# Optimization experiments

Hardware: AMD Instinct MI355X
Metric: run time of the kernel (lower is better)

## Reference

```python
import jax, jax.numpy as jnp
import numpy as np

ALPHA = 0.2  # LeakyReLU negative slope
NEG_INF = -9e15  # matches torch's -9000000000000000.0


def setup_inputs() -> dict:
    key = jax.random.key(0)
    k1, k2, k3, k4 = jax.random.split(key, 4)
    B, T, N, F_in, D = 4, 32, 512, 128, 128
    h = jax.random.normal(k1, (B, T, N, F_in), dtype=jnp.float32)
    adj = jax.random.randint(k2, (N, N), 0, 2, dtype=jnp.int32)
    # params: W ~ Linear(in_dim, out_dim, bias=False); a ~ Linear(2*out_dim, 1, bias=False)
    W = jax.random.normal(k3, (F_in, D), dtype=jnp.float32) * 0.05
    a = jax.random.normal(k4, (2 * D,), dtype=jnp.float32) * 0.05
    return {"h": h, "adj": adj, "W": W, "a": a}


def reference(h, adj, W, a):
    # h: (B,T,N,F_in), adj: (N,N), W: (F_in,D), a: (2D,)
    D = W.shape[1]
    Wh = jnp.einsum('btnf,fd->btnd', h, W)  # (B,T,N,D)
    # a . [Wh_i ; Wh_j] == a_src . Wh_i + a_dst . Wh_j -- avoids (N,N,2D) concat
    a_src, a_dst = a[:D], a[D:]
    e_src = Wh @ a_src  # (B,T,N)
    e_dst = Wh @ a_dst  # (B,T,N)
    e = jax.nn.leaky_relu(e_src[..., :, None] + e_dst[..., None, :], ALPHA)  # (B,T,N,N)
    e = jnp.where(adj > 0, e, jnp.float32(NEG_INF))
    attention = jax.nn.softmax(e, axis=-1)  # dropout is identity at eval
    h_prime = jnp.einsum('btij,btjd->btid', attention, Wh)  # (B,T,N,D)
    return h_prime
```

## Files before the change

kernel.cpp:

```cpp
#include <hip/hip_runtime.h>
#include <math.h>

typedef __attribute__((ext_vector_type(8))) short bf16x8;
typedef __attribute__((ext_vector_type(4))) float f32x4;

#define MFMA(a, b, c) __builtin_amdgcn_mfma_f32_16x16x32_bf16(a, b, c, 0, 0, 0)

constexpr int GN = 128;
constexpr int NN = 512;
constexpr int FD = 128;
#define LOG2E 1.4426950408889634f

__device__ inline unsigned rne_top16(float x) {
    unsigned u = __float_as_uint(x);
    return u + 0x7fffu + ((u >> 16) & 1u);
}
__device__ inline unsigned pack_top16(unsigned e1, unsigned e0) {
    return __builtin_amdgcn_perm(e1, e0, 0x07060302u);
}
__device__ inline void gload16(const void* g, void* l) {
    __builtin_amdgcn_global_load_lds(
        (const __attribute__((address_space(1))) unsigned*)g,
        (__attribute__((address_space(3))) unsigned*)l, 16, 0, 0);
}

__global__ __launch_bounds__(256, 2) void whb_kernel(
    const float* __restrict__ h, const float* __restrict__ a,
    const int* __restrict__ adj, const float* __restrict__ W,
    unsigned short* __restrict__ whtHi,
    float* __restrict__ esrc, float* __restrict__ edst,
    unsigned* __restrict__ mask)
{
    __shared__ __attribute__((aligned(16))) unsigned short sW[32768];

    const int bid = blockIdx.x;
    const int xcd = bid & 7, slot = bid >> 3;
    const int g = xcd + 8 * (slot >> 2);
    const int jt = slot & 3;
    const int t = threadIdx.x, lane = t & 63, w = t >> 6;
    const int i0r = jt * 128;
    const int q8 = (lane >> 4) * 8;
    const float* hg = h + (size_t)(g * NN) * FD;

    float4 hv[16];
    #pragma unroll
    for (int kk = 0; kk < 4; ++kk)
        #pragma unroll
        for (int mt = 0; mt < 2; ++mt) {
            const float* src = hg + (size_t)(i0r + w * 32 + mt * 16 + (lane & 15)) * FD
                             + kk * 32 + q8;
            hv[(kk * 2 + mt) * 2 + 0] = *(const float4*)src;
            hv[(kk * 2 + mt) * 2 + 1] = *(const float4*)(src + 4);
        }

    {
        const int pred0 = adj[bid * NN + t] > 0;
        const int pred1 = adj[bid * NN + 256 + t] > 0;
        const unsigned long long m0 = __ballot(pred0);
        const unsigned long long m1 = __ballot(pred1);
        if (lane == 0) {
            mask[bid * 16 + 2 * w]     = (unsigned)m0;
            mask[bid * 16 + 8 + 2 * w] = (unsigned)m1;
        } else if (lane == 1) {
            mask[bid * 16 + 2 * w + 1]     = (unsigned)(m0 >> 32);
            mask[bid * 16 + 8 + 2 * w + 1] = (unsigned)(m1 >> 32);
        }
    }

    #pragma unroll
    for (int grp = 0; grp < 8; ++grp) {
        const int p8 = grp * 256 + t;
        const int lanep = p8 & 63, cn = p8 >> 6;
        const int kks = cn >> 3, nbs = cn & 7;
        const int kbase = kks * 32 + ((lanep >> 4) & 3) * 8;
        const int d = nbs * 16 + (lanep & 15);
        unsigned hi[8], lo[8];
        #pragma unroll
        for (int idx = 0; idx < 8; ++idx) {
            const float wv = W[(kbase + idx) * FD + d];
            const unsigned u = __float_as_uint(wv);
            hi[idx] = u;
            lo[idx] = rne_top16(wv - __uint_as_float(u & 0xffff0000u));
        }
        uint4 H4, L4;
        H4.x = pack_top16(hi[1], hi[0]); H4.y = pack_top16(hi[3], hi[2]);
        H4.z = pack_top16(hi[5], hi[4]); H4.w = pack_top16(hi[7], hi[6]);
        L4.x = pack_top16(lo[1], lo[0]); L4.y = pack_top16(lo[3], lo[2]);
        L4.z = pack_top16(lo[5], lo[4]); L4.w = pack_top16(lo[7], lo[6]);
        *(uint4*)&sW[p8 * 8]         = H4;
        *(uint4*)&sW[16384 + p8 * 8] = L4;
    }
    __syncthreads();

    f32x4 acc[2][8];
    #pragma unroll
    for (int mt = 0; mt < 2; ++mt)
        #pragma unroll
        for (int nb = 0; nb < 8; ++nb) acc[mt][nb] = (f32x4){0.f, 0.f, 0.f, 0.f};

    #pragma unroll
    for (int kk = 0; kk < 4; ++kk) {
        bf16x8 ah[2], al[2];
        #pragma unroll
        for (int mt = 0; mt < 2; ++mt) {
            const float4 f0 = hv[(kk * 2 + mt) * 2 + 0];
            const float4 f1 = hv[(kk * 2 + mt) * 2 + 1];
            const float xs[8] = {f0.x, f0.y, f0.z, f0.w, f1.x, f1.y, f1.z, f1.w};
            union { bf16x8 v; unsigned u[4]; } H, L;
            #pragma unroll
            for (int j = 0; j < 4; ++j) {
                const unsigned e0 = __float_as_uint(xs[2 * j]);
                const unsigned e1 = __float_as_uint(xs[2 * j + 1]);
                H.u[j] = pack_top16(e1, e0);
                const unsigned l0 = rne_top16(xs[2*j]   - __uint_as_float(e0 & 0xffff0000u));
                const unsigned l1 = rne_top16(xs[2*j+1] - __uint_as_float(e1 & 0xffff0000u));
                L.u[j] = pack_top16(l1, l0);
            }
            ah[mt] = H.v; al[mt] = L.v;
        }
        #pragma unroll
        for (int nb = 0; nb < 8; ++nb) {
            const bf16x8 bh = *(const bf16x8*)&sW[((kk * 8 + nb) * 64 + lane) * 8];
            const bf16x8 bl = *(const bf16x8*)&sW[16384 + ((kk * 8 + nb) * 64 + lane) * 8];
            #pragma unroll
            for (int mt = 0; mt < 2; ++mt) {
                acc[mt][nb] = MFMA(al[mt], bh, acc[mt][nb]);
                acc[mt][nb] = MFMA(ah[mt], bl, acc[mt][nb]);
                acc[mt][nb] = MFMA(ah[mt], bh, acc[mt][nb]);
            }
        }
    }

    float av[8], bv[8];
    #pragma unroll
    for (int nb = 0; nb < 8; ++nb) {
        av[nb] = a[nb * 16 + (lane & 15)];
        bv[nb] = a[FD + nb * 16 + (lane & 15)];
    }
    #pragma unroll
    for (int mt = 0; mt < 2; ++mt)
        #pragma unroll
        for (int r = 0; r < 4; ++r) {
            float ps = 0.f, pd = 0.f;
            #pragma unroll
            for (int nb = 0; nb < 8; ++nb) {
                ps += acc[mt][nb][r] * av[nb];
                pd += acc[mt][nb][r] * bv[nb];
            }
            #pragma unroll
            for (int off = 1; off <= 8; off <<= 1) {
                ps += __shfl_xor(ps, off);
                pd += __shfl_xor(pd, off);
            }
            if ((lane & 15) == 0) {
                const int row = g * NN + i0r + w * 32 + mt * 16 + (lane >> 4) * 4 + r;
                esrc[row] = ps;
                edst[row] = pd;
            }
        }

    unsigned short* sT = sW;
    const size_t gbase = (size_t)g * 65536 + (size_t)jt * 16384;
    const int ib = 4 * ((lane >> 4) & 1);

    __syncthreads();
    #pragma unroll
    for (int mt = 0; mt < 2; ++mt) {
        const int lp2 = (lane & 15) + 16 * (mt * 2 + (lane >> 5));
        #pragma unroll
        for (int nb = 0; nb < 8; ++nb) {
            const int off = ((w * 8 + nb) * 64 + lp2) * 8 + ib;
            const unsigned r0 = rne_top16(acc[mt][nb][0]);
            const unsigned r1 = rne_top16(acc[mt][nb][1]);
            const unsigned r2 = rne_top16(acc[mt][nb][2]);
            const unsigned r3 = rne_top16(acc[mt][nb][3]);
            *(uint2*)&sT[off] = make_uint2(pack_top16(r1, r0), pack_top16(r3, r2));
        }
    }
    __syncthreads();
    for (int q = t; q < 2048; q += 256)
        *(float4*)&whtHi[gbase + q * 8] = *(const float4*)&sT[q * 8];
}

__global__ __launch_bounds__(256, 2) void attn_kernel(
    const unsigned short* __restrict__ whtHi,
    const float* __restrict__ esrc, const float* __restrict__ edst,
    const unsigned* __restrict__ mask, float* __restrict__ out)
{
    __shared__ __attribute__((aligned(16))) float eds[NN];
    __shared__ unsigned maskS[128 * 17];
    __shared__ __attribute__((aligned(16))) unsigned short cHi[2][8192];

    const int bid = blockIdx.x;
    const int xcd = bid & 7, slot = bid >> 3;
    const int g = xcd + 8 * (slot >> 2);
    const int it = slot & 3;
    const int t = threadIdx.x, lane = t & 63, w = t >> 6;
    const int i0 = it * 128;
    const int q8 = (lane >> 4) * 8;
    const int l15 = lane & 15;

    eds[t]       = edst[g * NN + t] * LOG2E;
    eds[t + 256] = edst[g * NN + 256 + t] * LOG2E;
    for (int q = t; q < 2048; q += 256) {
        const int row = q >> 4, wo = q & 15;
        maskS[row * 17 + wo] = mask[(i0 + row) * 16 + wo];
    }

    const int rloc0 = w * 32 + l15;
    const int rloc1 = rloc0 + 16;
    const float s0 = esrc[g * NN + i0 + rloc0] * LOG2E;
    const float s1 = esrc[g * NN + i0 + rloc1] * LOG2E;

    union { bf16x8 v; unsigned short s[8]; } bo;
    {
        const unsigned short oneb = (l15 == 0) ? (unsigned short)0x3f80 : (unsigned short)0;
        #pragma unroll
        for (int j = 0; j < 8; ++j) bo.s[j] = oneb;
    }

    const size_t gbase = (size_t)g * 65536;
    for (int q = t; q < 1024; q += 256)
        gload16(&whtHi[gbase + q * 8], &cHi[0][q * 8]);
    __syncthreads();

    f32x4 acc[2][8];
    #pragma unroll
    for (int mt = 0; mt < 2; ++mt)
        #pragma unroll
        for (int nb = 0; nb < 8; ++nb) acc[mt][nb] = (f32x4){0.f, 0.f, 0.f, 0.f};
    f32x4 accS0 = (f32x4){0.f, 0.f, 0.f, 0.f};
    f32x4 accS1 = (f32x4){0.f, 0.f, 0.f, 0.f};

    for (int c2 = 0; c2 < 8; ++c2) {
        const int cur = c2 & 1, nxt = cur ^ 1;
        if (c2 < 7) {
            const size_t gb = gbase + (size_t)(c2 + 1) * 8192;
            for (int q = t; q < 1024; q += 256)
                gload16(&whtHi[gb + q * 8], &cHi[nxt][q * 8]);
        }
        const unsigned short* __restrict__ bHi = &cHi[cur][0];
        #pragma unroll
        for (int kl = 0; kl < 2; ++kl) {
            const int kk = c2 * 2 + kl;
            const float* ep = &eds[kk * 32 + q8];
            const float4 ed0 = *(const float4*)ep;
            const float4 ed1 = *(const float4*)(ep + 4);
            const float ev[8] = {ed0.x, ed0.y, ed0.z, ed0.w, ed1.x, ed1.y, ed1.z, ed1.w};
            const unsigned mw0 = maskS[rloc0 * 17 + kk] >> q8;
            const unsigned mw1 = maskS[rloc1 * 17 + kk] >> q8;

            union { bf16x8 v; unsigned u[4]; } H0, H1;
            unsigned uh0[8], uh1[8];
            #pragma unroll
            for (int i = 0; i < 8; ++i) {
                const float z0 = s0 + ev[i];
                float p0 = __builtin_amdgcn_exp2f(fmaxf(z0, 0.2f * z0));
                p0 = ((mw0 >> i) & 1u) ? p0 : 0.f;
                uh0[i] = __float_as_uint(p0);
                const float z1 = s1 + ev[i];
                float p1 = __builtin_amdgcn_exp2f(fmaxf(z1, 0.2f * z1));
                p1 = ((mw1 >> i) & 1u) ? p1 : 0.f;
                uh1[i] = __float_as_uint(p1);
            }
            #pragma unroll
            for (int j = 0; j < 4; ++j) {
                H0.u[j] = pack_top16(uh0[2*j+1], uh0[2*j]);
                H1.u[j] = pack_top16(uh1[2*j+1], uh1[2*j]);
            }
            #pragma unroll
            for (int nb = 0; nb < 8; ++nb) {
                const bf16x8 bh = *(const bf16x8*)&bHi[((kl * 8 + nb) * 64 + lane) * 8];
                acc[0][nb] = MFMA(H0.v, bh, acc[0][nb]);
                acc[1][nb] = MFMA(H1.v, bh, acc[1][nb]);
            }
            accS0 = MFMA(H0.v, bo.v, accS0);
            accS1 = MFMA(H1.v, bo.v, accS1);
        }
        __syncthreads();
    }

    #pragma unroll
    for (int r = 0; r < 4; ++r) {
        const float rl0 = 1.0f / __shfl(accS0[r], lane & 48);
        const float rl1 = 1.0f / __shfl(accS1[r], lane & 48);
        const int row0 = g * NN + i0 + w * 32 + (lane >> 4) * 4 + r;
        const int row1 = row0 + 16;
        #pragma unroll
        for (int nb = 0; nb < 8; ++nb) {
            out[row0 * FD + nb * 16 + l15] = acc[0][nb][r] * rl0;
            out[row1 * FD + nb * 16 + l15] = acc[1][nb][r] * rl1;
        }
    }
}

extern "C" void kernel_launch(void* const* d_in, const int* in_sizes, int n_in,
                              void* d_out, int out_size, void* d_ws, size_t ws_size,
                              hipStream_t stream) {
    const float* h   = (const float*)d_in[0];
    const int*   adj = (const int*)d_in[1];
    const float* W   = (const float*)d_in[2];
    const float* a   = (const float*)d_in[3];
    float* out = (float*)d_out;

    unsigned short* whtHi = (unsigned short*)d_ws;
    float* esrc = (float*)(whtHi + (size_t)GN * 65536);
    float* edst = esrc + GN * NN;
    unsigned* mask = (unsigned*)(edst + GN * NN);

    whb_kernel<<<512, 256, 0, stream>>>(h, a, adj, W, whtHi, esrc, edst, mask);
    attn_kernel<<<512, 256, 0, stream>>>(whtHi, esrc, edst, mask, out);
}
```

Before: 113.8 us.

## Fuse projection and attention into one kernel with the Wh tile held in LDS

Replaces the two-kernel pipeline with one 512-thread kernel. Each block recomputes the full Wh projection for its graph, keeps it in LDS as bf16 together with the e_src and e_dst scores, then computes attention for half of the rows. The goal is to remove the global round-trip of the bf16 Wh tensor and the score arrays, the separate mask-packing step, and the second launch. In exchange, every graph's projection is computed twice. The adjacency is also read directly as int4 from global memory on every pass. The large LDS footprint (about 148KB) limits the GPU to one block per CU.

```diff
diff --git a/kernel.cpp b/kernel.cpp
--- a/kernel.cpp
+++ b/kernel.cpp
@@ -18,93 +18,69 @@
 __device__ inline unsigned pack_top16(unsigned e1, unsigned e0) {
     return __builtin_amdgcn_perm(e1, e0, 0x07060302u);
 }
-__device__ inline void gload16(const void* g, void* l) {
-    __builtin_amdgcn_global_load_lds(
-        (const __attribute__((address_space(1))) unsigned*)g,
-        (__attribute__((address_space(3))) unsigned*)l, 16, 0, 0);
-}
-
-__global__ __launch_bounds__(256, 2) void whb_kernel(
+
+__global__ __launch_bounds__(512, 2) void gat_fused_kernel(
     const float* __restrict__ h, const float* __restrict__ a,
     const int* __restrict__ adj, const float* __restrict__ W,
-    unsigned short* __restrict__ whtHi,
-    float* __restrict__ esrc, float* __restrict__ edst,
-    unsigned* __restrict__ mask)
+    float* __restrict__ out)
 {
-    __shared__ __attribute__((aligned(16))) unsigned short sW[32768];
+    __shared__ __attribute__((aligned(16))) unsigned short sWh[65536];
+    __shared__ __attribute__((aligned(16))) unsigned short sWc[8192];
+    __shared__ __attribute__((aligned(16))) float sEsrc[NN];
+    __shared__ __attribute__((aligned(16))) float sEdst[NN];
 
     const int bid = blockIdx.x;
     const int xcd = bid & 7, slot = bid >> 3;
-    const int g = xcd + 8 * (slot >> 2);
-    const int jt = slot & 3;
+    const int g  = xcd * 16 + (slot >> 1);
+    const int hf = slot & 1;
     const int t = threadIdx.x, lane = t & 63, w = t >> 6;
-    const int i0r = jt * 128;
-    const int q8 = (lane >> 4) * 8;
-    const float* hg = h + (size_t)(g * NN) * FD;
-
-    float4 hv[16];
-    #pragma unroll
-    for (int kk = 0; kk < 4; ++kk)
-        #pragma unroll
-        for (int mt = 0; mt < 2; ++mt) {
-            const float* src = hg + (size_t)(i0r + w * 32 + mt * 16 + (lane & 15)) * FD
+    const int l15 = lane & 15, q8 = (lane >> 4) * 8;
+    const float* hg = h + (size_t)g * NN * FD;
+
+    f32x4 acc1[4][8];
+    #pragma unroll
+    for (int mt = 0; mt < 4; ++mt)
+        #pragma unroll
+        for (int nb = 0; nb < 8; ++nb) acc1[mt][nb] = (f32x4){0.f, 0.f, 0.f, 0.f};
+
+    const int sd = w * 16 + l15;
+
+    #pragma unroll
+    for (int kk = 0; kk < 4; ++kk) {
+        float4 hv[8];
+        #pragma unroll
+        for (int mt = 0; mt < 4; ++mt) {
+            const float* src = hg + (size_t)(w * 64 + mt * 16 + l15) * FD
                              + kk * 32 + q8;
-            hv[(kk * 2 + mt) * 2 + 0] = *(const float4*)src;
-            hv[(kk * 2 + mt) * 2 + 1] = *(const float4*)(src + 4);
-        }
-
-    {
-        const int pred0 = adj[bid * NN + t] > 0;
-        const int pred1 = adj[bid * NN + 256 + t] > 0;
-        const unsigned long long m0 = __ballot(pred0);
-        const unsigned long long m1 = __ballot(pred1);
-        if (lane == 0) {
-            mask[bid * 16 + 2 * w]     = (unsigned)m0;
-            mask[bid * 16 + 8 + 2 * w] = (unsigned)m1;
-        } else if (lane == 1) {
-            mask[bid * 16 + 2 * w + 1]     = (unsigned)(m0 >> 32);
-            mask[bid * 16 + 8 + 2 * w + 1] = (unsigned)(m1 >> 32);
-        }
-    }
-
-    #pragma unroll
-    for (int grp = 0; grp < 8; ++grp) {
-        const int p8 = grp * 256 + t;
-        const int lanep = p8 & 63, cn = p8 >> 6;
-        const int kks = cn >> 3, nbs = cn & 7;
-        const int kbase = kks * 32 + ((lanep >> 4) & 3) * 8;
-        const int d = nbs * 16 + (lanep & 15);
-        unsigned hi[8], lo[8];
-        #pragma unroll
-        for (int idx = 0; idx < 8; ++idx) {
-            const float wv = W[(kbase + idx) * FD + d];
-            const unsigned u = __float_as_uint(wv);
-            hi[idx] = u;
-            lo[idx] = rne_top16(wv - __uint_as_float(u & 0xffff0000u));
-        }
-        uint4 H4, L4;
-        H4.x = pack_top16(hi[1], hi[0]); H4.y = pack_top16(hi[3], hi[2]);
-        H4.z = pack_top16(hi[5], hi[4]); H4.w = pack_top16(hi[7], hi[6]);
-        L4.x = pack_top16(lo[1], lo[0]); L4.y = pack_top16(lo[3], lo[2]);
-        L4.z = pack_top16(lo[5], lo[4]); L4.w = pack_top16(lo[7], lo[6]);
-        *(uint4*)&sW[p8 * 8]         = H4;
-        *(uint4*)&sW[16384 + p8 * 8] = L4;
-    }
-    __syncthreads();
-
-    f32x4 acc[2][8];
-    #pragma unroll
-    for (int mt = 0; mt < 2; ++mt)
-        #pragma unroll
-        for (int nb = 0; nb < 8; ++nb) acc[mt][nb] = (f32x4){0.f, 0.f, 0.f, 0.f};
-
-    #pragma unroll
-    for (int kk = 0; kk < 4; ++kk) {
-        bf16x8 ah[2], al[2];
-        #pragma unroll
-        for (int mt = 0; mt < 2; ++mt) {
-            const float4 f0 = hv[(kk * 2 + mt) * 2 + 0];
-            const float4 f1 = hv[(kk * 2 + mt) * 2 + 1];
+            hv[2 * mt]     = *(const float4*)src;
+            hv[2 * mt + 1] = *(const float4*)(src + 4);
+        }
+
+        if (kk > 0) __syncthreads();
+        {
+            const int kbase = kk * 32 + q8;
+            unsigned hi[8], lo[8];
+            #pragma unroll
+            for (int idx = 0; idx < 8; ++idx) {
+                const float wv = W[(kbase + idx) * FD + sd];
+                const unsigned u = __float_as_uint(wv);
+                hi[idx] = u;
+                lo[idx] = rne_top16(wv - __uint_as_float(u & 0xffff0000u));
+            }
+            uint4 H4, L4;
+            H4.x = pack_top16(hi[1], hi[0]); H4.y = pack_top16(hi[3], hi[2]);
+            H4.z = pack_top16(hi[5], hi[4]); H4.w = pack_top16(hi[7], hi[6]);
+            L4.x = pack_top16(lo[1], lo[0]); L4.y = pack_top16(lo[3], lo[2]);
+            L4.z = pack_top16(lo[5], lo[4]); L4.w = pack_top16(lo[7], lo[6]);
+            *(uint4*)&sWc[t * 8]        = H4;
+            *(uint4*)&sWc[4096 + t * 8] = L4;
+        }
+        __syncthreads();
+
+        bf16x8 ah[4], al[4];
+        #pragma unroll
+        for (int mt = 0; mt < 4; ++mt) {
+            const float4 f0 = hv[2 * mt], f1 = hv[2 * mt + 1];
             const float xs[8] = {f0.x, f0.y, f0.z, f0.w, f1.x, f1.y, f1.z, f1.w};
             union { bf16x8 v; unsigned u[4]; } H, L;
             #pragma unroll
@@ -120,97 +96,73 @@
         }
         #pragma unroll
         for (int nb = 0; nb < 8; ++nb) {
-            const bf16x8 bh = *(const bf16x8*)&sW[((kk * 8 + nb) * 64 + lane) * 8];
-            const bf16x8 bl = *(const bf16x8*)&sW[16384 + ((kk * 8 + nb) * 64 + lane) * 8];
-            #pragma unroll
-            for (int mt = 0; mt < 2; ++mt) {
-                acc[mt][nb] = MFMA(al[mt], bh, acc[mt][nb]);
-                acc[mt][nb] = MFMA(ah[mt], bl, acc[mt][nb]);
-                acc[mt][nb] = MFMA(ah[mt], bh, acc[mt][nb]);
-            }
-        }
-    }
-
-    float av[8], bv[8];
-    #pragma unroll
-    for (int nb = 0; nb < 8; ++nb) {
-        av[nb] = a[nb * 16 + (lane & 15)];
-        bv[nb] = a[FD + nb * 16 + (lane & 15)];
-    }
-    #pragma unroll
-    for (int mt = 0; mt < 2; ++mt)
-        #pragma unroll
-        for (int r = 0; r < 4; ++r) {
-            float ps = 0.f, pd = 0.f;
+            const bf16x8 bh = *(const bf16x8*)&sWc[(nb * 64 + lane) * 8];
+            const bf16x8 bl = *(const bf16x8*)&sWc[4096 + (nb * 64 + lane) * 8];
+            #pragma unroll
+            for (int mt = 0; mt < 4; ++mt) {
+                acc1[mt][nb] = MFMA(al[mt], bh, acc1[mt][nb]);
+                acc1[mt][nb] = MFMA(ah[mt], bl, acc1[mt][nb]);
+                acc1[mt][nb] = MFMA(ah[mt], bh, acc1[mt][nb]);
+            }
+        }
+    }
+
+    {
+        float av[8], bv[8];
+        #pragma unroll
+        for (int nb = 0; nb < 8; ++nb) {
+            av[nb] = a[nb * 16 + l15];
+            bv[nb] = a[FD + nb * 16 + l15];
+        }
+        #pragma unroll
+        for (int mt = 0; mt < 4; ++mt)
+            #pragma unroll
+            for (int r = 0; r < 4; ++r) {
+                float ps = 0.f, pd = 0.f;
+                #pragma unroll
+                for (int nb = 0; nb < 8; ++nb) {
+                    ps += acc1[mt][nb][r] * av[nb];
+                    pd += acc1[mt][nb][r] * bv[nb];
+                }
+                #pragma unroll
+                for (int off = 1; off <= 8; off <<= 1) {
+                    ps += __shfl_xor(ps, off);
+                    pd += __shfl_xor(pd, off);
+                }
+                if (l15 == 0) {
+                    const int row = w * 64 + mt * 16 + (lane >> 4) * 4 + r;
+                    sEsrc[row] = ps * LOG2E;
+                    sEdst[row] = pd * LOG2E;
+                }
+            }
+    }
+
+    {
+        const int ib = 4 * ((lane >> 4) & 1);
+        #pragma unroll
+        for (int mt = 0; mt < 4; ++mt) {
+            const int KK = w * 2 + (mt >> 1);
+            const int lp2 = l15 + 16 * ((mt & 1) * 2 + (lane >> 5));
             #pragma unroll
             for (int nb = 0; nb < 8; ++nb) {
-                ps += acc[mt][nb][r] * av[nb];
-                pd += acc[mt][nb][r] * bv[nb];
-            }
-            #pragma unroll
-            for (int off = 1; off <= 8; off <<= 1) {
-                ps += __shfl_xor(ps, off);
-                pd += __shfl_xor(pd, off);
-            }
-            if ((lane & 15) == 0) {
-                const int row = g * NN + i0r + w * 32 + mt * 16 + (lane >> 4) * 4 + r;
-                esrc[row] = ps;
-                edst[row] = pd;
-            }
-        }
-
-    unsigned short* sT = sW;
-    const size_t gbase = (size_t)g * 65536 + (size_t)jt * 16384;
-    const int ib = 4 * ((lane >> 4) & 1);
-
+                const int off = ((KK * 8 + nb) * 64 + lp2) * 8 + ib;
+                const unsigned r0 = rne_top16(acc1[mt][nb][0]);
+                const unsigned r1 = rne_top16(acc1[mt][nb][1]);
+                const unsigned r2 = rne_top16(acc1[mt][nb][2]);
+                const unsigned r3 = rne_top16(acc1[mt][nb][3]);
+                *(uint2*)&sWh[off] = make_uint2(pack_top16(r1, r0), pack_top16(r3, r2));
+            }
+        }
+    }
     __syncthreads();
-    #pragma unroll
-    for (int mt = 0; mt < 2; ++mt) {
-        const int lp2 = (lane & 15) + 16 * (mt * 2 + (lane >> 5));
-        #pragma unroll
-        for (int nb = 0; nb < 8; ++nb) {
-            const int off = ((w * 8 + nb) * 64 + lp2) * 8 + ib;
-            const unsigned r0 = rne_top16(acc[mt][nb][0]);
-            const unsigned r1 = rne_top16(acc[mt][nb][1]);
-            const unsigned r2 = rne_top16(acc[mt][nb][2]);
-            const unsigned r3 = rne_top16(acc[mt][nb][3]);
-            *(uint2*)&sT[off] = make_uint2(pack_top16(r1, r0), pack_top16(r3, r2));
-        }
-    }
-    __syncthreads();
-    for (int q = t; q < 2048; q += 256)
-        *(float4*)&whtHi[gbase + q * 8] = *(const float4*)&sT[q * 8];
-}
-
-__global__ __launch_bounds__(256, 2) void attn_kernel(
-    const unsigned short* __restrict__ whtHi,
-    const float* __restrict__ esrc, const float* __restrict__ edst,
-    const unsigned* __restrict__ mask, float* __restrict__ out)
-{
-    __shared__ __attribute__((aligned(16))) float eds[NN];
-    __shared__ unsigned maskS[128 * 17];
-    __shared__ __attribute__((aligned(16))) unsigned short cHi[2][8192];
-
-    const int bid = blockIdx.x;
-    const int xcd = bid & 7, slot = bid >> 3;
-    const int g = xcd + 8 * (slot >> 2);
-    const int it = slot & 3;
-    const int t = threadIdx.x, lane = t & 63, w = t >> 6;
-    const int i0 = it * 128;
-    const int q8 = (lane >> 4) * 8;
-    const int l15 = lane & 15;
-
-    eds[t]       = edst[g * NN + t] * LOG2E;
-    eds[t + 256] = edst[g * NN + 256 + t] * LOG2E;
-    for (int q = t; q < 2048; q += 256) {
-        const int row = q >> 4, wo = q & 15;
-        maskS[row * 17 + wo] = mask[(i0 + row) * 16 + wo];
-    }
 
     const int rloc0 = w * 32 + l15;
-    const int rloc1 = rloc0 + 16;
-    const float s0 = esrc[g * NN + i0 + rloc0] * LOG2E;
-    const float s1 = esrc[g * NN + i0 + rloc1] * LOG2E;
+    const int irow0 = hf * 256 + rloc0;
+    const int irow1 = irow0 + 16;
+    const float s0 = sEsrc[irow0];
+    const float s1 = sEsrc[irow1];
+    const int* adjr0 = adj + (size_t)irow0 * NN;
+    const int* adjr1 = adj + (size_t)irow1 * NN;
 
     union { bf16x8 v; unsigned short s[8]; } bo;
     {
@@ -219,11 +171,6 @@
         for (int j = 0; j < 8; ++j) bo.s[j] = oneb;
     }
 
-    const size_t gbase = (size_t)g * 65536;
-    for (int q = t; q < 1024; q += 256)
-        gload16(&whtHi[gbase + q * 8], &cHi[0][q * 8]);
-    __syncthreads();
-
     f32x4 acc[2][8];
     #pragma unroll
     for (int mt = 0; mt < 2; ++mt)
@@ -232,59 +179,61 @@
     f32x4 accS0 = (f32x4){0.f, 0.f, 0.f, 0.f};
     f32x4 accS1 = (f32x4){0.f, 0.f, 0.f, 0.f};
 
-    for (int c2 = 0; c2 < 8; ++c2) {
-        const int cur = c2 & 1, nxt = cur ^ 1;
-        if (c2 < 7) {
-            const size_t gb = gbase + (size_t)(c2 + 1) * 8192;
-            for (int q = t; q < 1024; q += 256)
-                gload16(&whtHi[gb + q * 8], &cHi[nxt][q * 8]);
-        }
-        const unsigned short* __restrict__ bHi = &cHi[cur][0];
-        #pragma unroll
-        for (int kl = 0; kl < 2; ++kl) {
-            const int kk = c2 * 2 + kl;
-            const float* ep = &eds[kk * 32 + q8];
-            const float4 ed0 = *(const float4*)ep;
-            const float4 ed1 = *(const float4*)(ep + 4);
-            const float ev[8] = {ed0.x, ed0.y, ed0.z, ed0.w, ed1.x, ed1.y, ed1.z, ed1.w};
-            const unsigned mw0 = maskS[rloc0 * 17 + kk] >> q8;
-            const unsigned mw1 = maskS[rloc1 * 17 + kk] >> q8;
-
-            union { bf16x8 v; unsigned u[4]; } H0, H1;
-            unsigned uh0[8], uh1[8];
-            #pragma unroll
-            for (int i = 0; i < 8; ++i) {
-                const float z0 = s0 + ev[i];
-                float p0 = __builtin_amdgcn_exp2f(fmaxf(z0, 0.2f * z0));
-                p0 = ((mw0 >> i) & 1u) ? p0 : 0.f;
-                uh0[i] = __float_as_uint(p0);
-                const float z1 = s1 + ev[i];
-                float p1 = __builtin_amdgcn_exp2f(fmaxf(z1, 0.2f * z1));
-                p1 = ((mw1 >> i) & 1u) ? p1 : 0.f;
-                uh1[i] = __float_as_uint(p1);
-            }
-            #pragma unroll
-            for (int j = 0; j < 4; ++j) {
-                H0.u[j] = pack_top16(uh0[2*j+1], uh0[2*j]);
-                H1.u[j] = pack_top16(uh1[2*j+1], uh1[2*j]);
-            }
-            #pragma unroll
-            for (int nb = 0; nb < 8; ++nb) {
-                const bf16x8 bh = *(const bf16x8*)&bHi[((kl * 8 + nb) * 64 + lane) * 8];
-                acc[0][nb] = MFMA(H0.v, bh, acc[0][nb]);
-                acc[1][nb] = MFMA(H1.v, bh, acc[1][nb]);
-            }
-            accS0 = MFMA(H0.v, bo.v, accS0);
-            accS1 = MFMA(H1.v, bo.v, accS1);
-        }
-        __syncthreads();
+    int4 n00 = *(const int4*)&adjr0[q8];
+    int4 n01 = *(const int4*)&adjr0[q8 + 4];
+    int4 n10 = *(const int4*)&adjr1[q8];
+    int4 n11 = *(const int4*)&adjr1[q8 + 4];
+
+    for (int KK = 0; KK < 16; ++KK) {
+        const int4 m00 = n00, m01 = n01, m10 = n10, m11 = n11;
+        if (KK < 15) {
+            const int jb = (KK + 1) * 32 + q8;
+            n00 = *(const int4*)&adjr0[jb];
+            n01 = *(const int4*)&adjr0[jb + 4];
+            n10 = *(const int4*)&adjr1[jb];
+            n11 = *(const int4*)&adjr1[jb + 4];
+        }
+        const float* ep = &sEdst[KK * 32 + q8];
+        const float4 ed0 = *(const float4*)ep;
+        const float4 ed1 = *(const float4*)(ep + 4);
+        const float ev[8] = {ed0.x, ed0.y, ed0.z, ed0.w, ed1.x, ed1.y, ed1.z, ed1.w};
+        int ma0[8], ma1[8];
+        *(int4*)&ma0[0] = m00; *(int4*)&ma0[4] = m01;
+        *(int4*)&ma1[0] = m10; *(int4*)&ma1[4] = m11;
+
+        union { bf16x8 v; unsigned u[4]; } H0, H1;
+        unsigned uh0[8], uh1[8];
+        #pragma unroll
+        for (int i = 0; i < 8; ++i) {
+            const float z0 = s0 + ev[i];
+            float p0 = __builtin_amdgcn_exp2f(fmaxf(z0, 0.2f * z0));
+            p0 = (ma0[i] > 0) ? p0 : 0.f;
+            uh0[i] = __float_as_uint(p0);
+            const float z1 = s1 + ev[i];
+            float p1 = __builtin_amdgcn_exp2f(fmaxf(z1, 0.2f * z1));
+            p1 = (ma1[i] > 0) ? p1 : 0.f;
+            uh1[i] = __float_as_uint(p1);
+        }
+        #pragma unroll
+        for (int j = 0; j < 4; ++j) {
+            H0.u[j] = pack_top16(uh0[2*j+1], uh0[2*j]);
+            H1.u[j] = pack_top16(uh1[2*j+1], uh1[2*j]);
+        }
+        #pragma unroll
+        for (int nb = 0; nb < 8; ++nb) {
+            const bf16x8 bh = *(const bf16x8*)&sWh[((KK * 8 + nb) * 64 + lane) * 8];
+            acc[0][nb] = MFMA(H0.v, bh, acc[0][nb]);
+            acc[1][nb] = MFMA(H1.v, bh, acc[1][nb]);
+        }
+        accS0 = MFMA(H0.v, bo.v, accS0);
+        accS1 = MFMA(H1.v, bo.v, accS1);
     }
 
     #pragma unroll
     for (int r = 0; r < 4; ++r) {
         const float rl0 = 1.0f / __shfl(accS0[r], lane & 48);
         const float rl1 = 1.0f / __shfl(accS1[r], lane & 48);
-        const int row0 = g * NN + i0 + w * 32 + (lane >> 4) * 4 + r;
+        const int row0 = g * NN + hf * 256 + w * 32 + (lane >> 4) * 4 + r;
         const int row1 = row0 + 16;
         #pragma unroll
         for (int nb = 0; nb < 8; ++nb) {
@@ -302,12 +251,7 @@
     const float* W   = (const float*)d_in[2];
     const float* a   = (const float*)d_in[3];
     float* out = (float*)d_out;
-
-    unsigned short* whtHi = (unsigned short*)d_ws;
-    float* esrc = (float*)(whtHi + (size_t)GN * 65536);
-    float* edst = esrc + GN * NN;
-    unsigned* mask = (unsigned*)(edst + GN * NN);
-
-    whb_kernel<<<512, 256, 0, stream>>>(h, a, adj, W, whtHi, esrc, edst, mask);
-    attn_kernel<<<512, 256, 0, stream>>>(whtHi, esrc, edst, mask, out);
-}
+    (void)d_ws; (void)ws_size;
+
+    gat_fused_kernel<<<256, 512, 0, stream>>>(h, a, adj, W, out);
+}
```

New measurement: 117.4 us. +3.2%, slower.
